# Optimization experiments

Measured on AMD Instinct MI355X. Metric: run time of the kernel, lower is better.

Reference implementation:

```python
import jax, jax.numpy as jnp
import numpy as np

SIGMA = 0.2


def setup_inputs() -> dict:
    key = jax.random.key(0)
    ks = jax.random.split(key, 16)
    N = 200000
    corner = jax.random.normal(ks[0], (N, 9), dtype=jnp.float32)
    normal = jax.random.normal(ks[1], (N, 3), dtype=jnp.float32)
    neighbour = jax.random.randint(ks[2], (N, 3), 0, N, dtype=jnp.int32)
    # Face_Rotate_Conv params: Conv1d(1,32,6,stride=3), Linear(32,64), Linear(64,64)
    conv_w = jax.random.normal(ks[3], (32, 1, 6), dtype=jnp.float32) * 0.3
    conv_b = jax.random.normal(ks[4], (32,), dtype=jnp.float32) * 0.1
    l3_w = jax.random.normal(ks[5], (64, 32), dtype=jnp.float32) * 0.15
    l3_b = jax.random.normal(ks[6], (64,), dtype=jnp.float32) * 0.05
    l4_w = jax.random.normal(ks[7], (64, 64), dtype=jnp.float32) * 0.12
    l4_b = jax.random.normal(ks[8], (64,), dtype=jnp.float32) * 0.05
    # Kernel_Correlation params: theta ~ U(0,pi), phi ~ U(0,2pi), shape [1,64,4]
    theta = jax.random.uniform(ks[9], (1, 64, 4), dtype=jnp.float32) * np.float32(np.pi)
    phi = jax.random.uniform(ks[10], (1, 64, 4), dtype=jnp.float32) * np.float32(2 * np.pi)
    # trailing 1x1 conv / bn / 1x1 conv on 131 channels
    c1_w = jax.random.normal(ks[11], (131, 131, 1), dtype=jnp.float32) * 0.08
    c1_b = jax.random.normal(ks[12], (131,), dtype=jnp.float32) * 0.05
    c2_w = jax.random.normal(ks[13], (131, 131, 1), dtype=jnp.float32) * 0.08
    c2_b = jax.random.normal(ks[14], (131,), dtype=jnp.float32) * 0.05
    bn_g = jnp.ones((131,), dtype=jnp.float32)
    bn_b = jnp.zeros((131,), dtype=jnp.float32)
    return {"corner": corner, "normal": normal, "neighbour": neighbour,
            "conv_w": conv_w, "conv_b": conv_b, "l3_w": l3_w, "l3_b": l3_b,
            "l4_w": l4_w, "l4_b": l4_b, "theta": theta, "phi": phi,
            "c1_w": c1_w, "c1_b": c1_b, "c2_w": c2_w, "c2_b": c2_b,
            "bn_g": bn_g, "bn_b": bn_b}


def reference(corner, normal, neighbour, conv_w, conv_b, l3_w, l3_b, l4_w, l4_b,
              theta, phi, c1_w, c1_b, c2_w, c2_b, bn_g, bn_b):
    # ---- Face_Rotate_Conv ----
    # cat(c1,c2,c3,c1) -> [n,12]; conv1d k=6 stride=3 over length 12 -> 3 windows
    arr = jnp.concatenate([corner[:, 0:3], corner[:, 3:6], corner[:, 6:9], corner[:, 0:3]], axis=1)
    patches = jnp.stack([arr[:, 0:6], arr[:, 3:9], arr[:, 6:12]], axis=1)  # [n,3,6]
    conv_out = jnp.einsum('npk,ok->npo', patches, conv_w[:, 0, :]) + conv_b  # [n,3,32]
    frc = conv_out.mean(axis=1)  # [n,32] (mean over output length == mean over windows)
    h = jax.nn.relu(frc @ l3_w.T + l3_b)
    x = h @ l4_w.T + l4_b  # [n,64]
    # ---- Kernel_Correlation ----
    nb = neighbour.astype(jnp.int32)
    f = jnp.stack([normal, normal[nb[:, 0]], normal[nb[:, 1]], normal[nb[:, 2]]], axis=2)  # [n,3,4]
    th, ph = theta[0], phi[0]  # [64,4]
    kern = jnp.stack([jnp.sin(th) * jnp.sin(ph), jnp.sin(th) * jnp.cos(ph), jnp.cos(th)], axis=0)  # [3,64,4]
    # ||f - k||^2 over xyz expanded via |f|^2 + |k|^2 - 2 f.k (avoids [n,3,64,4,4])
    f2 = jnp.sum(f * f, axis=1)   # [n,4]
    k2 = jnp.sum(kern * kern, axis=0)  # [64,4]
    cross = jnp.einsum('nca,cmb->nmab', f, kern)  # [n,64,4,4]
    correl = f2[:, None, :, None] + k2[None, :, None, :] - 2.0 * cross
    z = jnp.exp(correl / (-2.0 * SIGMA * SIGMA)).sum(axis=(2, 3)) / 16.0  # [n,64]
    # ---- structural_Des head ----
    feat = jnp.concatenate([normal, x, z], axis=1)  # [n,131]
    y = feat @ c1_w[:, :, 0].T + c1_b  # 1x1 conv == linear
    mu = y.mean(axis=0)
    var = y.var(axis=0)  # biased var, matches train-mode BatchNorm1d
    y = jax.nn.relu((y - mu) / jnp.sqrt(var + 1e-5) * bn_g + bn_b)
    out = y @ c2_w[:, :, 0].T + c2_b
    return out  # [n,131]
```

## Files before the change

kernel.cpp:

```cpp
#include <hip/hip_runtime.h>
#include <math.h>

typedef __attribute__((ext_vector_type(8))) short short8;
typedef _Float16 half8 __attribute__((ext_vector_type(8)));
typedef __attribute__((ext_vector_type(4))) float f32x4;
typedef __attribute__((ext_vector_type(2))) uint uint2v;
typedef unsigned int uint;
typedef unsigned short ushort;

#define N_PTS 200000
#define N_PAD 200064
#define NBLK  1563
#define NPAIR 6252
#define YST   168
#define ZK    (-18.033688011112043f)
#define C2K   (36.067376022224086f)


#define FEAT_OFF  0ull
#define WT1_OFF   118437888ull
#define WT2_OFF   118483968ull
#define KERN2_OFF 118530048ull
#define WSUM_OFF  118534144ull
#define L3H_OFF   118534528ull
#define L4H_OFF   118538624ull
#define GSUM_OFF  118546816ull
#define GSQ_OFF   118547456ull
#define SCALE_OFF 118548096ull
#define SHIFT_OFF 118548736ull

__device__ inline ushort f2h(float x) {
    return __builtin_bit_cast(ushort, (_Float16)x);
}
__device__ inline uint pack2h(float a, float b) {
    return __builtin_bit_cast(uint, __builtin_amdgcn_cvt_pkrtz(a, b));
}

__global__ void sdes_k0_setup(const float* __restrict__ conv_w, const float* __restrict__ l3w,
                              const float* __restrict__ l4w, const float* __restrict__ theta,
                              const float* __restrict__ phi, const float* __restrict__ c1w,
                              const float* __restrict__ c2w,
                              float* wsumT, ushort* l3h, ushort* l4h, float* kern2,
                              ushort* WT1t, ushort* WT2t, float* gsum, float* gsq)
{
    const int t = threadIdx.x, b = blockIdx.x;
    if (b == 90) {
        for (int i = t; i < 96; i += 256) {
            int k = i >> 5, o = i & 31;
            wsumT[k * 32 + o] = conv_w[o * 6 + k] + conv_w[o * 6 + k + 3];
        }
        for (int i = t; i < 2048; i += 256) l3h[i] = f2h(l3w[i]);
        for (int i = t; i < 4096; i += 256) l4h[i] = f2h(l4w[i]);
        int m = t >> 2, bb = t & 3;
        float th = theta[m * 4 + bb], ph = phi[m * 4 + bb];
        float st = sinf(th), ct = cosf(th), sp = sinf(ph), cp = cosf(ph);
        kern2[m * 16 + bb * 4 + 0] = st * sp * C2K;
        kern2[m * 16 + bb * 4 + 1] = st * cp * C2K;
        kern2[m * 16 + bb * 4 + 2] = ct * C2K;
        kern2[m * 16 + bb * 4 + 3] = 0.f;
        return;
    }
    if (b == 0 && t < 160) { gsum[t] = 0.f; gsq[t] = 0.f; }
    int i = b * 256 + t;
    if (i >= 144 * 160) return;
    int e = i & 7, l = (i >> 3) & 63, rem = i >> 9;
    int kc = rem % 5, tc = rem / 5;
    int n = tc * 16 + (l & 15);
    int k = kc * 32 + (l >> 4) * 8 + e;
    float v = 0.f;
    if (n < 131) {
        if (k < 64)       v = c1w[n * 131 + 3 + k];
        else if (k < 128) v = c1w[n * 131 + 67 + (k - 64)];
        else if (k < 131) v = c1w[n * 131 + (k - 128)];
    }
    WT1t[i] = f2h(v);
    float v2 = (n < 131 && k < 131) ? c2w[n * 131 + k] : 0.f;
    WT2t[i] = f2h(v2);
}

#define FST 40
#define W3T 40
#define W4T 72
__global__ __launch_bounds__(128) void sdes_k1a_mlp(
    const float* __restrict__ corner, const float* __restrict__ conv_b,
    const float* __restrict__ wsumT, const ushort* __restrict__ l3h,
    const float* __restrict__ l3b, const ushort* __restrict__ l4h,
    const float* __restrict__ l4b, ushort* __restrict__ feat)
{
    __shared__ __align__(16) ushort frcS[128 * FST];
    __shared__ __align__(16) ushort hS[128 * 64];
    __shared__ __align__(16) ushort w3S[64 * W3T];
    __shared__ __align__(16) ushort w4S[64 * W4T];
    __shared__ float wsL[96], cbL[32], b3L[64], b4L[64];
    const int t = threadIdx.x;
    for (int i = t; i < 96; i += 128) wsL[i] = wsumT[i];
    for (int i = t; i < 32; i += 128) cbL[i] = conv_b[i];
    for (int i = t; i < 64; i += 128) { b3L[i] = l3b[i]; b4L[i] = l4b[i]; }
    for (int i = t; i < 256; i += 128) {
        int c = i >> 2, kc = i & 3;
        *(uint4*)&w3S[c * W3T + kc * 8] = *(const uint4*)&l3h[c * 32 + kc * 8];
    }
    for (int i = t; i < 512; i += 128) {
        int c = i >> 3, kc = i & 7;
        *(uint4*)&w4S[c * W4T + kc * 8] = *(const uint4*)&l4h[c * 64 + kc * 8];
    }
    __syncthreads();
    {
        int row = blockIdx.x * 128 + t;
        int p = row < N_PTS ? row : N_PTS - 1;
        const float* cp = corner + (size_t)p * 9;
        float c0 = cp[0], c1 = cp[1], c2 = cp[2], c3 = cp[3], c4 = cp[4],
              c5 = cp[5], c6 = cp[6], c7 = cp[7], c8 = cp[8];
        float mp0 = (c0 + c3 + c6) * (1.f / 3.f);
        float mp1 = (c1 + c4 + c7) * (1.f / 3.f);
        float mp2 = (c2 + c5 + c8) * (1.f / 3.f);
        #pragma unroll
        for (int o = 0; o < 32; o += 2) {
            float f0 = fmaf(mp0, wsL[o], fmaf(mp1, wsL[32 + o], fmaf(mp2, wsL[64 + o], cbL[o])));
            float f1 = fmaf(mp0, wsL[o+1], fmaf(mp1, wsL[33 + o], fmaf(mp2, wsL[65 + o], cbL[o+1])));
            *(uint*)&frcS[t * FST + o] = pack2h(f0, f1);
        }
    }
    __syncthreads();

    const int lane = t & 63, w = t >> 6;
    const int rbase = w * 64;
    const int rlo = lane & 15, kg = lane >> 4;
    const f32x4 z4 = {0.f, 0.f, 0.f, 0.f};

    {
        half8 af[4], bf[4];
        #pragma unroll
        for (int rt = 0; rt < 4; ++rt)
            af[rt] = *(const half8*)&frcS[(rbase + rt * 16 + rlo) * FST + kg * 8];
        #pragma unroll
        for (int tc = 0; tc < 4; ++tc)
            bf[tc] = *(const half8*)&w3S[(tc * 16 + rlo) * W3T + kg * 8];
        #pragma unroll
        for (int rt = 0; rt < 4; ++rt) {
            #pragma unroll
            for (int tc = 0; tc < 4; ++tc) {
                f32x4 acc = __builtin_amdgcn_mfma_f32_16x16x32_f16(af[rt], bf[tc], z4, 0, 0, 0);
                int col = tc * 16 + rlo;
                float bias = b3L[col];
                #pragma unroll
                for (int r = 0; r < 4; ++r) {
                    int hrow = rbase + rt * 16 + kg * 4 + r;
                    float v = fmaxf(acc[r] + bias, 0.f);
                    int sc = (((col >> 3) ^ (hrow & 7)) << 3) | (col & 7);
                    hS[hrow * 64 + sc] = f2h(v);
                }
            }
        }
    }
    __syncthreads();

    f32x4 acc4[4][4];
    #pragma unroll
    for (int pt = 0; pt < 4; ++pt)
        #pragma unroll
        for (int tc = 0; tc < 4; ++tc) acc4[pt][tc] = z4;
    #pragma unroll
    for (int ks = 0; ks < 2; ++ks) {
        half8 af[4], bf[4];
        #pragma unroll
        for (int pt = 0; pt < 4; ++pt) {
            int row = rbase + pt * 16 + rlo;
            int blk = (ks * 4 + kg) ^ (rlo & 7);
            af[pt] = *(const half8*)&hS[row * 64 + blk * 8];
        }
        #pragma unroll
        for (int tc = 0; tc < 4; ++tc)
            bf[tc] = *(const half8*)&w4S[(tc * 16 + rlo) * W4T + ks * 32 + kg * 8];
        #pragma unroll
        for (int pt = 0; pt < 4; ++pt)
            #pragma unroll
            for (int tc = 0; tc < 4; ++tc)
                acc4[pt][tc] = __builtin_amdgcn_mfma_f32_16x16x32_f16(bf[tc], af[pt], acc4[pt][tc], 0, 0, 0);
    }
    #pragma unroll
    for (int pt = 0; pt < 4; ++pt) {
        int rtg = blockIdx.x * 8 + w * 4 + pt;
        #pragma unroll
        for (int tc = 0; tc < 4; ++tc) {
            int xb = tc * 16 + kg * 4;
            float v0 = acc4[pt][tc][0] + b4L[xb + 0];
            float v1 = acc4[pt][tc][1] + b4L[xb + 1];
            float v2 = acc4[pt][tc][2] + b4L[xb + 2];
            float v3 = acc4[pt][tc][3] + b4L[xb + 3];
            uint2v st; st.x = pack2h(v0, v1); st.y = pack2h(v2, v3);
            int kc = tc >> 1;
            int l = rlo + 16 * ((2 * tc + (kg >> 1)) & 3);
            size_t off = ((size_t)(rtg * 5 + kc)) * 512 + l * 8 + (kg & 1) * 4;
            *(uint2v*)(feat + off) = st;
        }
    }
}

__global__ __launch_bounds__(256) void sdes_k1b_z(
    const float* __restrict__ normal, const int* __restrict__ neigh,
    const float* __restrict__ kern2g, ushort* __restrict__ feat)
{
    const int t = threadIdx.x;
    const int tt = t >> 7;
    const int pi = t & 127;
    const int p0 = blockIdx.x * 128 + pi;
    const int p = p0 < N_PTS ? p0 : N_PTS - 1;
    const int rt = p0 >> 4, pl = p0 & 15;
    float f0[4], f1[4], f2v[4];
    f0[0] = normal[(size_t)p * 3 + 0]; f1[0] = normal[(size_t)p * 3 + 1]; f2v[0] = normal[(size_t)p * 3 + 2];
    #pragma unroll
    for (int a = 1; a < 4; ++a) {
        int nb = neigh[(size_t)p * 3 + (a - 1)];
        f0[a] = normal[(size_t)nb * 3 + 0];
        f1[a] = normal[(size_t)nb * 3 + 1];
        f2v[a] = normal[(size_t)nb * 3 + 2];
    }
    float base[4];
    #pragma unroll
    for (int a = 0; a < 4; ++a)
        base[a] = (f0[a]*f0[a] + f1[a]*f1[a] + f2v[a]*f2v[a] + 1.0f) * ZK;
    const size_t tbase = ((size_t)(rt * 5 + 2 + tt)) * 512;
    for (int qq = 0; qq < 4; ++qq) {
        float zv[8];
        #pragma unroll
        for (int mm = 0; mm < 8; ++mm) {
            int m = (tt * 4 + qq) * 8 + mm;
            const float* kp = kern2g + m * 16;
            float a0 = 0.f, a1 = 0.f, a2 = 0.f, a3 = 0.f;
            #pragma unroll
            for (int b = 0; b < 4; ++b) {
                float kx = kp[b * 4 + 0], ky = kp[b * 4 + 1], kz = kp[b * 4 + 2];
                a0 += __builtin_amdgcn_exp2f(fmaf(f0[0], kx, fmaf(f1[0], ky, fmaf(f2v[0], kz, base[0]))));
                a1 += __builtin_amdgcn_exp2f(fmaf(f0[1], kx, fmaf(f1[1], ky, fmaf(f2v[1], kz, base[1]))));
                a2 += __builtin_amdgcn_exp2f(fmaf(f0[2], kx, fmaf(f1[2], ky, fmaf(f2v[2], kz, base[2]))));
                a3 += __builtin_amdgcn_exp2f(fmaf(f0[3], kx, fmaf(f1[3], ky, fmaf(f2v[3], kz, base[3]))));
            }
            zv[mm] = ((a0 + a1) + (a2 + a3)) * (1.f / 16.f);
        }
        uint4 v;
        v.x = pack2h(zv[0], zv[1]); v.y = pack2h(zv[2], zv[3]);
        v.z = pack2h(zv[4], zv[5]); v.w = pack2h(zv[6], zv[7]);
        *(uint4*)(feat + tbase + (pl + 16 * qq) * 8) = v;
    }
    {
        size_t base4 = ((size_t)(rt * 5 + 4)) * 512;
        const uint4 zz = {0u, 0u, 0u, 0u};
        if (tt == 0) {
            uint4 v;
            v.x = pack2h(f0[0], f1[0]); v.y = pack2h(f2v[0], 0.f); v.z = 0u; v.w = 0u;
            *(uint4*)(feat + base4 + pl * 8) = v;
            *(uint4*)(feat + base4 + (pl + 16) * 8) = zz;
        } else {
            *(uint4*)(feat + base4 + (pl + 32) * 8) = zz;
            *(uint4*)(feat + base4 + (pl + 48) * 8) = zz;
        }
    }
}

__global__ __launch_bounds__(1024, 4) void sdes_k2_stats(
    const ushort* __restrict__ FT, const ushort* __restrict__ WT1t,
    const float* __restrict__ c1b, float* __restrict__ gsum, float* __restrict__ gsq)
{
    __shared__ __align__(16) ushort W1s[45 * 512];
    __shared__ float sS[144], sQ[144];
    const int t = threadIdx.x;
    const int lane = t & 63, wv = t >> 6;
    const int b = blockIdx.x;
    const int s = b * 16 + wv;
    const int rlo = lane & 15, kg = lane >> 4;

    const int cnt = 3 + ((wv == 0 && b < 216) ? 1 : 0);
    const int start = 3 * s + (b < 216 ? b : 216) + ((b < 216 && wv > 0) ? 1 : 0);

    half8 afA[5], afB[5];
    #pragma unroll
    for (int kc = 0; kc < 5; ++kc)
        afA[kc] = *(const half8*)(FT + ((size_t)start * 5 + kc) * 512 + lane * 8);

    for (int i = t; i < 2880; i += 1024) ((uint4*)W1s)[i] = ((const uint4*)WT1t)[i];
    if (t < 144) { sS[t] = 0.f; sQ[t] = 0.f; }
    __syncthreads();

    float sreg[9], qreg[9], bL[9];
    #pragma unroll
    for (int tc = 0; tc < 9; ++tc) {
        sreg[tc] = 0.f; qreg[tc] = 0.f;
        int n = tc * 16 + rlo;
        bL[tc] = (n < 131) ? c1b[n] : 0.f;
    }

    for (int it = 0; it < cnt; ++it) {
        const int p = start + it;
        f32x4 acc[9];
        #pragma unroll
        for (int tc = 0; tc < 9; ++tc) acc[tc] = (f32x4){0.f, 0.f, 0.f, 0.f};
        #pragma unroll
        for (int kc = 0; kc < 5; ++kc) {
            #pragma unroll
            for (int tc = 0; tc < 9; ++tc) {
                half8 bw = *(const half8*)(W1s + (tc * 5 + kc) * 512 + lane * 8);
                acc[tc] = __builtin_amdgcn_mfma_f32_16x16x32_f16(afA[kc], bw, acc[tc], 0, 0, 0);
            }
        }
        if (it + 1 < cnt) {
            #pragma unroll
            for (int kc = 0; kc < 5; ++kc)
                afB[kc] = *(const half8*)(FT + ((size_t)(p + 1) * 5 + kc) * 512 + lane * 8);
            __builtin_amdgcn_sched_barrier(0);
        }
        const int row0 = p * 16;
        #pragma unroll
        for (int tc = 0; tc < 9; ++tc) {
            float b0 = bL[tc];
            #pragma unroll
            for (int r = 0; r < 4; ++r) {
                int grow = row0 + kg * 4 + r;
                if (grow < N_PTS) {
                    float v = acc[tc][r] + b0;
                    sreg[tc] += v;
                    qreg[tc] = fmaf(v, v, qreg[tc]);
                }
            }
        }
        #pragma unroll
        for (int kc = 0; kc < 5; ++kc) afA[kc] = afB[kc];
    }

    #pragma unroll
    for (int tc = 0; tc < 9; ++tc) {
        float sv = sreg[tc], qv = qreg[tc];
        sv += __shfl_xor(sv, 16);  sv += __shfl_xor(sv, 32);
        qv += __shfl_xor(qv, 16);  qv += __shfl_xor(qv, 32);
        if (lane < 16) {
            int n = tc * 16 + rlo;
            atomicAdd(&sS[n], sv); atomicAdd(&sQ[n], qv);
        }
    }
    __syncthreads();
    if (t < 144) { atomicAdd(&gsum[t], sS[t]); atomicAdd(&gsq[t], sQ[t]); }
}

__global__ __launch_bounds__(768, 3) void sdes_k3_fused(
    const ushort* __restrict__ FT, const ushort* __restrict__ WT1t,
    const ushort* __restrict__ WT2t, const float* __restrict__ c1b,
    const float* __restrict__ gsum, const float* __restrict__ gsq,
    const float* __restrict__ bng, const float* __restrict__ bnb,
    const float* __restrict__ c2b, float* __restrict__ out)
{
    __shared__ __align__(16) ushort Ws[2 * 45 * 512];
    __shared__ __align__(16) ushort yS[192 * YST];
    __shared__ float scL[160], shL[160], b1L[160], c2L[160];
    const int t = threadIdx.x;
    const int lane = t & 63, wv = t >> 6;
    const int rlo = lane & 15, kg = lane >> 4;
    const int b = blockIdx.x;
    const int s = b * 12 + wv;

    const int cnt = 2 + ((wv == 0 && b < 108) ? 1 : 0);
    const int start = 2 * s + (b < 108 ? b : 108) + ((b < 108 && wv > 0) ? 1 : 0);

    half8 afA[5][2], afB[5][2];
    #pragma unroll
    for (int kc = 0; kc < 5; ++kc)
        #pragma unroll
        for (int pt = 0; pt < 2; ++pt)
            afA[kc][pt] = *(const half8*)(FT + ((size_t)(start * 2 + pt) * 5 + kc) * 512 + lane * 8);

    for (int i = t; i < 5760; i += 768) ((uint4*)Ws)[i] = ((const uint4*)WT1t)[i];

    if (t < 160) {
        float sc = 0.f, sh = 0.f, bb = 0.f, c2 = 0.f;
        if (t < 131) {
            float mu = gsum[t] * (1.f / 200000.f);
            float var = gsq[t] * (1.f / 200000.f) - mu * mu;
            sc = bng[t] / sqrtf(var + 1e-5f);
            sh = bnb[t] - mu * sc;
            bb = c1b[t]; c2 = c2b[t];
        }
        scL[t] = sc; shL[t] = sh; b1L[t] = bb; c2L[t] = c2;
    }
    __syncthreads();

    const half8 hz = {0, 0, 0, 0, 0, 0, 0, 0};
    ushort* slab = yS + wv * 16 * YST;

    for (int it = 0; it < cnt; ++it) {
        const int p = start + it;

        f32x4 acc[2][9];
        #pragma unroll
        for (int pt = 0; pt < 2; ++pt)
            #pragma unroll
            for (int tc = 0; tc < 9; ++tc) acc[pt][tc] = (f32x4){0.f, 0.f, 0.f, 0.f};
        #pragma unroll
        for (int kc = 0; kc < 5; ++kc) {
            #pragma unroll
            for (int tc = 0; tc < 9; ++tc) {
                half8 bw = *(const half8*)(Ws + (tc * 5 + kc) * 512 + lane * 8);
                #pragma unroll
                for (int pt = 0; pt < 2; ++pt)
                    acc[pt][tc] = __builtin_amdgcn_mfma_f32_16x16x32_f16(afA[kc][pt], bw, acc[pt][tc], 0, 0, 0);
            }
        }

        if (it + 1 < cnt) {
            #pragma unroll
            for (int kc = 0; kc < 5; ++kc)
                #pragma unroll
                for (int pt = 0; pt < 2; ++pt)
                    afB[kc][pt] = *(const half8*)(FT + ((size_t)((p + 1) * 2 + pt) * 5 + kc) * 512 + lane * 8);
            __builtin_amdgcn_sched_barrier(0);
        }

        const int row0 = p * 32;
        #pragma unroll
        for (int pt = 0; pt < 2; ++pt) {
            #pragma unroll
            for (int tc = 0; tc < 9; ++tc) {
                int n = tc * 16 + rlo;
                float sc = scL[n], sh = shL[n], bb = b1L[n];
                #pragma unroll
                for (int r = 0; r < 4; ++r) {
                    float v = fmaxf(fmaf(acc[pt][tc][r] + bb, sc, sh), 0.f);
                    slab[(kg * 4 + r) * YST + n] = f2h(v);
                }
            }

            f32x4 acc2[9];
            #pragma unroll
            for (int tc = 0; tc < 9; ++tc) acc2[tc] = (f32x4){0.f, 0.f, 0.f, 0.f};
            #pragma unroll
            for (int kc2 = 0; kc2 < 5; ++kc2) {
                bool vld = (kc2 < 4) || (kg < 2);
                half8 af2 = vld ? *(const half8*)&slab[rlo * YST + kc2 * 32 + kg * 8] : hz;
                #pragma unroll
                for (int tc = 0; tc < 9; ++tc) {
                    half8 bw = *(const half8*)(Ws + 23040 + (tc * 5 + kc2) * 512 + lane * 8);
                    acc2[tc] = __builtin_amdgcn_mfma_f32_16x16x32_f16(af2, bw, acc2[tc], 0, 0, 0);
                }
            }
            #pragma unroll
            for (int tc = 0; tc < 9; ++tc) {
                int n = tc * 16 + rlo;
                if (n < 131) {
                    float bias = c2L[n];
                    #pragma unroll
                    for (int r = 0; r < 4; ++r) {
                        int grow = row0 + pt * 16 + kg * 4 + r;
                        if (grow < N_PTS) out[(size_t)grow * 131 + n] = acc2[tc][r] + bias;
                    }
                }
            }
        }

        #pragma unroll
        for (int kc = 0; kc < 5; ++kc)
            #pragma unroll
            for (int pt = 0; pt < 2; ++pt)
                afA[kc][pt] = afB[kc][pt];
    }
}

extern "C" void kernel_launch(void* const* d_in, const int* in_sizes, int n_in,
                              void* d_out, int out_size, void* d_ws, size_t ws_size,
                              hipStream_t stream) {
    const float* corner = (const float*)d_in[0];
    const float* normal = (const float*)d_in[1];
    const int*   neigh  = (const int*)d_in[2];
    const float* conv_w = (const float*)d_in[3];
    const float* conv_b = (const float*)d_in[4];
    const float* l3_w   = (const float*)d_in[5];
    const float* l3_b   = (const float*)d_in[6];
    const float* l4_w   = (const float*)d_in[7];
    const float* l4_b   = (const float*)d_in[8];
    const float* theta  = (const float*)d_in[9];
    const float* phi    = (const float*)d_in[10];
    const float* c1_w   = (const float*)d_in[11];
    const float* c1_b   = (const float*)d_in[12];
    const float* c2_w   = (const float*)d_in[13];
    const float* c2_b   = (const float*)d_in[14];
    const float* bn_g   = (const float*)d_in[15];
    const float* bn_b   = (const float*)d_in[16];

    char* ws = (char*)d_ws;
    ushort* feat  = (ushort*)(ws + FEAT_OFF);
    ushort* WT1t  = (ushort*)(ws + WT1_OFF);
    ushort* WT2t  = (ushort*)(ws + WT2_OFF);
    float*  kern2 = (float*)(ws + KERN2_OFF);
    float*  wsumT = (float*)(ws + WSUM_OFF);
    ushort* l3h   = (ushort*)(ws + L3H_OFF);
    ushort* l4h   = (ushort*)(ws + L4H_OFF);
    float*  gsum  = (float*)(ws + GSUM_OFF);
    float*  gsq   = (float*)(ws + GSQ_OFF);

    sdes_k0_setup<<<91, 256, 0, stream>>>(conv_w, l3_w, l4_w, theta, phi, c1_w, c2_w,
                                          wsumT, l3h, l4h, kern2, WT1t, WT2t, gsum, gsq);
    sdes_k1a_mlp<<<NBLK, 128, 0, stream>>>(corner, conv_b, wsumT, l3h, l3_b, l4h, l4_b, feat);
    sdes_k1b_z<<<NBLK, 256, 0, stream>>>(normal, neigh, kern2, feat);
    sdes_k2_stats<<<256, 1024, 0, stream>>>(feat, WT1t, c1_b, gsum, gsq);
    sdes_k3_fused<<<256, 768, 0, stream>>>(feat, WT1t, WT2t, c1_b, gsum, gsq,
                                           bn_g, bn_b, c2_b, (float*)d_out);
}
```

Before: 139.1 us.

## Fuse MLP and correlation kernels, store pre-BN activations instead of recomputing first GEMM

Merges the face-MLP and kernel-correlation kernels into one 256-thread launch, with half the threads doing only the exp-based correlation while two waves run the MFMA layers. The stats kernel now writes the first linear layer's output in fp16 to a workspace buffer. The final kernel reads that buffer, applies batch norm and ReLU in registers, and runs only the second GEMM, so it no longer recomputes the first GEMM. The c2 bias is folded into the weight matrix through a constant-1 column. This trades the recomputation for roughly 64 MB of extra global write and read traffic, and y is now rounded to fp16 before normalisation.

```diff
diff --git a/kernel.cpp b/kernel.cpp
--- a/kernel.cpp
+++ b/kernel.cpp
@@ -11,8 +11,7 @@
 #define N_PTS 200000
 #define N_PAD 200064
 #define NBLK  1563
-#define NPAIR 6252
-#define YST   168
+#define YRST  160
 #define ZK    (-18.033688011112043f)
 #define C2K   (36.067376022224086f)
 
@@ -26,8 +25,7 @@
 #define L4H_OFF   118538624ull
 #define GSUM_OFF  118546816ull
 #define GSQ_OFF   118547456ull
-#define SCALE_OFF 118548096ull
-#define SHIFT_OFF 118548736ull
+#define Y_OFF     118550528ull
 
 __device__ inline ushort f2h(float x) {
     return __builtin_bit_cast(ushort, (_Float16)x);
@@ -39,7 +37,7 @@
 __global__ void sdes_k0_setup(const float* __restrict__ conv_w, const float* __restrict__ l3w,
                               const float* __restrict__ l4w, const float* __restrict__ theta,
                               const float* __restrict__ phi, const float* __restrict__ c1w,
-                              const float* __restrict__ c2w,
+                              const float* __restrict__ c2w, const float* __restrict__ c2b,
                               float* wsumT, ushort* l3h, ushort* l4h, float* kern2,
                               ushort* WT1t, ushort* WT2t, float* gsum, float* gsq)
 {
@@ -74,18 +72,24 @@
         else if (k < 131) v = c1w[n * 131 + (k - 128)];
     }
     WT1t[i] = f2h(v);
-    float v2 = (n < 131 && k < 131) ? c2w[n * 131 + k] : 0.f;
+    float v2 = 0.f;
+    if (n < 131) {
+        if (k < 131)       v2 = c2w[n * 131 + k];
+        else if (k == 144) v2 = c2b[n];
+    }
     WT2t[i] = f2h(v2);
 }
 
 #define FST 40
 #define W3T 40
 #define W4T 72
-__global__ __launch_bounds__(128) void sdes_k1a_mlp(
+__global__ __launch_bounds__(256) void sdes_k1ab(
     const float* __restrict__ corner, const float* __restrict__ conv_b,
     const float* __restrict__ wsumT, const ushort* __restrict__ l3h,
     const float* __restrict__ l3b, const ushort* __restrict__ l4h,
-    const float* __restrict__ l4b, ushort* __restrict__ feat)
+    const float* __restrict__ l4b,
+    const float* __restrict__ normal, const int* __restrict__ neigh,
+    const float* __restrict__ kern2g, ushort* __restrict__ feat)
 {
     __shared__ __align__(16) ushort frcS[128 * FST];
     __shared__ __align__(16) ushort hS[128 * 64];
@@ -93,19 +97,21 @@
     __shared__ __align__(16) ushort w4S[64 * W4T];
     __shared__ float wsL[96], cbL[32], b3L[64], b4L[64];
     const int t = threadIdx.x;
-    for (int i = t; i < 96; i += 128) wsL[i] = wsumT[i];
-    for (int i = t; i < 32; i += 128) cbL[i] = conv_b[i];
-    for (int i = t; i < 64; i += 128) { b3L[i] = l3b[i]; b4L[i] = l4b[i]; }
-    for (int i = t; i < 256; i += 128) {
+
+    for (int i = t; i < 96; i += 256) wsL[i] = wsumT[i];
+    for (int i = t; i < 32; i += 256) cbL[i] = conv_b[i];
+    for (int i = t; i < 64; i += 256) { b3L[i] = l3b[i]; b4L[i] = l4b[i]; }
+    for (int i = t; i < 256; i += 256) {
         int c = i >> 2, kc = i & 3;
         *(uint4*)&w3S[c * W3T + kc * 8] = *(const uint4*)&l3h[c * 32 + kc * 8];
     }
-    for (int i = t; i < 512; i += 128) {
+    for (int i = t; i < 512; i += 256) {
         int c = i >> 3, kc = i & 7;
         *(uint4*)&w4S[c * W4T + kc * 8] = *(const uint4*)&l4h[c * 64 + kc * 8];
     }
     __syncthreads();
-    {
+
+    if (t < 128) {
         int row = blockIdx.x * 128 + t;
         int p = row < N_PTS ? row : N_PTS - 1;
         const float* cp = corner + (size_t)p * 9;
@@ -121,14 +127,71 @@
             *(uint*)&frcS[t * FST + o] = pack2h(f0, f1);
         }
     }
+
+    {
+        const int tt = t >> 7;
+        const int pi = t & 127;
+        const int p0 = blockIdx.x * 128 + pi;
+        const int p = p0 < N_PTS ? p0 : N_PTS - 1;
+        const int rt = p0 >> 4, pl = p0 & 15;
+        float f0[4], f1[4], f2v[4];
+        f0[0] = normal[(size_t)p * 3 + 0]; f1[0] = normal[(size_t)p * 3 + 1]; f2v[0] = normal[(size_t)p * 3 + 2];
+        #pragma unroll
+        for (int a = 1; a < 4; ++a) {
+            int nb = neigh[(size_t)p * 3 + (a - 1)];
+            f0[a] = normal[(size_t)nb * 3 + 0];
+            f1[a] = normal[(size_t)nb * 3 + 1];
+            f2v[a] = normal[(size_t)nb * 3 + 2];
+        }
+        float base[4];
+        #pragma unroll
+        for (int a = 0; a < 4; ++a)
+            base[a] = (f0[a]*f0[a] + f1[a]*f1[a] + f2v[a]*f2v[a] + 1.0f) * ZK;
+        const size_t tbase = ((size_t)(rt * 5 + 2 + tt)) * 512;
+        for (int qq = 0; qq < 4; ++qq) {
+            float zv[8];
+            #pragma unroll
+            for (int mm = 0; mm < 8; ++mm) {
+                int m = (tt * 4 + qq) * 8 + mm;
+                const float* kp = kern2g + m * 16;
+                float a0 = 0.f, a1 = 0.f, a2 = 0.f, a3 = 0.f;
+                #pragma unroll
+                for (int b = 0; b < 4; ++b) {
+                    float kx = kp[b * 4 + 0], ky = kp[b * 4 + 1], kz = kp[b * 4 + 2];
+                    a0 += __builtin_amdgcn_exp2f(fmaf(f0[0], kx, fmaf(f1[0], ky, fmaf(f2v[0], kz, base[0]))));
+                    a1 += __builtin_amdgcn_exp2f(fmaf(f0[1], kx, fmaf(f1[1], ky, fmaf(f2v[1], kz, base[1]))));
+                    a2 += __builtin_amdgcn_exp2f(fmaf(f0[2], kx, fmaf(f1[2], ky, fmaf(f2v[2], kz, base[2]))));
+                    a3 += __builtin_amdgcn_exp2f(fmaf(f0[3], kx, fmaf(f1[3], ky, fmaf(f2v[3], kz, base[3]))));
+                }
+                zv[mm] = ((a0 + a1) + (a2 + a3)) * (1.f / 16.f);
+            }
+            uint4 v;
+            v.x = pack2h(zv[0], zv[1]); v.y = pack2h(zv[2], zv[3]);
+            v.z = pack2h(zv[4], zv[5]); v.w = pack2h(zv[6], zv[7]);
+            *(uint4*)(feat + tbase + (pl + 16 * qq) * 8) = v;
+        }
+        {
+            size_t base4 = ((size_t)(rt * 5 + 4)) * 512;
+            const uint4 zz = {0u, 0u, 0u, 0u};
+            if (tt == 0) {
+                uint4 v;
+                v.x = pack2h(f0[0], f1[0]); v.y = pack2h(f2v[0], 0.f); v.z = 0u; v.w = 0u;
+                *(uint4*)(feat + base4 + pl * 8) = v;
+                *(uint4*)(feat + base4 + (pl + 16) * 8) = zz;
+            } else {
+                *(uint4*)(feat + base4 + (pl + 32) * 8) = zz;
+                *(uint4*)(feat + base4 + (pl + 48) * 8) = zz;
+            }
+        }
+    }
     __syncthreads();
 
     const int lane = t & 63, w = t >> 6;
-    const int rbase = w * 64;
     const int rlo = lane & 15, kg = lane >> 4;
     const f32x4 z4 = {0.f, 0.f, 0.f, 0.f};
 
-    {
+    if (w < 2) {
+        const int rbase = w * 64;
         half8 af[4], bf[4];
         #pragma unroll
         for (int rt = 0; rt < 4; ++rt)
@@ -155,112 +218,55 @@
     }
     __syncthreads();
 
-    f32x4 acc4[4][4];
-    #pragma unroll
-    for (int pt = 0; pt < 4; ++pt)
-        #pragma unroll
-        for (int tc = 0; tc < 4; ++tc) acc4[pt][tc] = z4;
-    #pragma unroll
-    for (int ks = 0; ks < 2; ++ks) {
-        half8 af[4], bf[4];
+    if (w < 2) {
+        const int rbase = w * 64;
+        f32x4 acc4[4][4];
+        #pragma unroll
+        for (int pt = 0; pt < 4; ++pt)
+            #pragma unroll
+            for (int tc = 0; tc < 4; ++tc) acc4[pt][tc] = z4;
+        #pragma unroll
+        for (int ks = 0; ks < 2; ++ks) {
+            half8 af[4], bf[4];
+            #pragma unroll
+            for (int pt = 0; pt < 4; ++pt) {
+                int row = rbase + pt * 16 + rlo;
+                int blk = (ks * 4 + kg) ^ (rlo & 7);
+                af[pt] = *(const half8*)&hS[row * 64 + blk * 8];
+            }
+            #pragma unroll
+            for (int tc = 0; tc < 4; ++tc)
+                bf[tc] = *(const half8*)&w4S[(tc * 16 + rlo) * W4T + ks * 32 + kg * 8];
+            #pragma unroll
+            for (int pt = 0; pt < 4; ++pt)
+                #pragma unroll
+                for (int tc = 0; tc < 4; ++tc)
+                    acc4[pt][tc] = __builtin_amdgcn_mfma_f32_16x16x32_f16(bf[tc], af[pt], acc4[pt][tc], 0, 0, 0);
+        }
         #pragma unroll
         for (int pt = 0; pt < 4; ++pt) {
-            int row = rbase + pt * 16 + rlo;
-            int blk = (ks * 4 + kg) ^ (rlo & 7);
-            af[pt] = *(const half8*)&hS[row * 64 + blk * 8];
-        }
-        #pragma unroll
-        for (int tc = 0; tc < 4; ++tc)
-            bf[tc] = *(const half8*)&w4S[(tc * 16 + rlo) * W4T + ks * 32 + kg * 8];
-        #pragma unroll
-        for (int pt = 0; pt < 4; ++pt)
-            #pragma unroll
-            for (int tc = 0; tc < 4; ++tc)
-                acc4[pt][tc] = __builtin_amdgcn_mfma_f32_16x16x32_f16(bf[tc], af[pt], acc4[pt][tc], 0, 0, 0);
-    }
-    #pragma unroll
-    for (int pt = 0; pt < 4; ++pt) {
-        int rtg = blockIdx.x * 8 + w * 4 + pt;
-        #pragma unroll
-        for (int tc = 0; tc < 4; ++tc) {
-            int xb = tc * 16 + kg * 4;
-            float v0 = acc4[pt][tc][0] + b4L[xb + 0];
-            float v1 = acc4[pt][tc][1] + b4L[xb + 1];
-            float v2 = acc4[pt][tc][2] + b4L[xb + 2];
-            float v3 = acc4[pt][tc][3] + b4L[xb + 3];
-            uint2v st; st.x = pack2h(v0, v1); st.y = pack2h(v2, v3);
-            int kc = tc >> 1;
-            int l = rlo + 16 * ((2 * tc + (kg >> 1)) & 3);
-            size_t off = ((size_t)(rtg * 5 + kc)) * 512 + l * 8 + (kg & 1) * 4;
-            *(uint2v*)(feat + off) = st;
-        }
-    }
-}
-
-__global__ __launch_bounds__(256) void sdes_k1b_z(
-    const float* __restrict__ normal, const int* __restrict__ neigh,
-    const float* __restrict__ kern2g, ushort* __restrict__ feat)
-{
-    const int t = threadIdx.x;
-    const int tt = t >> 7;
-    const int pi = t & 127;
-    const int p0 = blockIdx.x * 128 + pi;
-    const int p = p0 < N_PTS ? p0 : N_PTS - 1;
-    const int rt = p0 >> 4, pl = p0 & 15;
-    float f0[4], f1[4], f2v[4];
-    f0[0] = normal[(size_t)p * 3 + 0]; f1[0] = normal[(size_t)p * 3 + 1]; f2v[0] = normal[(size_t)p * 3 + 2];
-    #pragma unroll
-    for (int a = 1; a < 4; ++a) {
-        int nb = neigh[(size_t)p * 3 + (a - 1)];
-        f0[a] = normal[(size_t)nb * 3 + 0];
-        f1[a] = normal[(size_t)nb * 3 + 1];
-        f2v[a] = normal[(size_t)nb * 3 + 2];
-    }
-    float base[4];
-    #pragma unroll
-    for (int a = 0; a < 4; ++a)
-        base[a] = (f0[a]*f0[a] + f1[a]*f1[a] + f2v[a]*f2v[a] + 1.0f) * ZK;
-    const size_t tbase = ((size_t)(rt * 5 + 2 + tt)) * 512;
-    for (int qq = 0; qq < 4; ++qq) {
-        float zv[8];
-        #pragma unroll
-        for (int mm = 0; mm < 8; ++mm) {
-            int m = (tt * 4 + qq) * 8 + mm;
-            const float* kp = kern2g + m * 16;
-            float a0 = 0.f, a1 = 0.f, a2 = 0.f, a3 = 0.f;
-            #pragma unroll
-            for (int b = 0; b < 4; ++b) {
-                float kx = kp[b * 4 + 0], ky = kp[b * 4 + 1], kz = kp[b * 4 + 2];
-                a0 += __builtin_amdgcn_exp2f(fmaf(f0[0], kx, fmaf(f1[0], ky, fmaf(f2v[0], kz, base[0]))));
-                a1 += __builtin_amdgcn_exp2f(fmaf(f0[1], kx, fmaf(f1[1], ky, fmaf(f2v[1], kz, base[1]))));
-                a2 += __builtin_amdgcn_exp2f(fmaf(f0[2], kx, fmaf(f1[2], ky, fmaf(f2v[2], kz, base[2]))));
-                a3 += __builtin_amdgcn_exp2f(fmaf(f0[3], kx, fmaf(f1[3], ky, fmaf(f2v[3], kz, base[3]))));
-            }
-            zv[mm] = ((a0 + a1) + (a2 + a3)) * (1.f / 16.f);
-        }
-        uint4 v;
-        v.x = pack2h(zv[0], zv[1]); v.y = pack2h(zv[2], zv[3]);
-        v.z = pack2h(zv[4], zv[5]); v.w = pack2h(zv[6], zv[7]);
-        *(uint4*)(feat + tbase + (pl + 16 * qq) * 8) = v;
-    }
-    {
-        size_t base4 = ((size_t)(rt * 5 + 4)) * 512;
-        const uint4 zz = {0u, 0u, 0u, 0u};
-        if (tt == 0) {
-            uint4 v;
-            v.x = pack2h(f0[0], f1[0]); v.y = pack2h(f2v[0], 0.f); v.z = 0u; v.w = 0u;
-            *(uint4*)(feat + base4 + pl * 8) = v;
-            *(uint4*)(feat + base4 + (pl + 16) * 8) = zz;
-        } else {
-            *(uint4*)(feat + base4 + (pl + 32) * 8) = zz;
-            *(uint4*)(feat + base4 + (pl + 48) * 8) = zz;
-        }
-    }
-}
-
-__global__ __launch_bounds__(1024, 4) void sdes_k2_stats(
+            int rtg = blockIdx.x * 8 + w * 4 + pt;
+            #pragma unroll
+            for (int tc = 0; tc < 4; ++tc) {
+                int xb = tc * 16 + kg * 4;
+                float v0 = acc4[pt][tc][0] + b4L[xb + 0];
+                float v1 = acc4[pt][tc][1] + b4L[xb + 1];
+                float v2 = acc4[pt][tc][2] + b4L[xb + 2];
+                float v3 = acc4[pt][tc][3] + b4L[xb + 3];
+                uint2v st; st.x = pack2h(v0, v1); st.y = pack2h(v2, v3);
+                int kc = tc >> 1;
+                int l = rlo + 16 * ((2 * tc + (kg >> 1)) & 3);
+                size_t off = ((size_t)(rtg * 5 + kc)) * 512 + l * 8 + (kg & 1) * 4;
+                *(uint2v*)(feat + off) = st;
+            }
+        }
+    }
+}
+
+__global__ __launch_bounds__(1024, 4) void sdes_k2y(
     const ushort* __restrict__ FT, const ushort* __restrict__ WT1t,
-    const float* __restrict__ c1b, float* __restrict__ gsum, float* __restrict__ gsq)
+    const float* __restrict__ c1b, float* __restrict__ gsum, float* __restrict__ gsq,
+    ushort* __restrict__ yH)
 {
     __shared__ __align__(16) ushort W1s[45 * 512];
     __shared__ float sS[144], sQ[144];
@@ -312,16 +318,24 @@
         const int row0 = p * 16;
         #pragma unroll
         for (int tc = 0; tc < 9; ++tc) {
+            const int n = tc * 16 + rlo;
             float b0 = bL[tc];
             #pragma unroll
             for (int r = 0; r < 4; ++r) {
                 int grow = row0 + kg * 4 + r;
+                float v = acc[tc][r] + b0;
+                yH[(size_t)grow * YRST + n] = f2h(v);
                 if (grow < N_PTS) {
-                    float v = acc[tc][r] + b0;
                     sreg[tc] += v;
                     qreg[tc] = fmaf(v, v, qreg[tc]);
                 }
             }
+        }
+        {
+            uint2v pz;
+            pz.x = (kg == 0) ? pack2h(1.f, 0.f) : 0u;
+            pz.y = 0u;
+            *(uint2v*)(yH + (size_t)(row0 + rlo) * YRST + 144 + kg * 4) = pz;
         }
         #pragma unroll
         for (int kc = 0; kc < 5; ++kc) afA[kc] = afB[kc];
@@ -341,124 +355,86 @@
     if (t < 144) { atomicAdd(&gsum[t], sS[t]); atomicAdd(&gsq[t], sQ[t]); }
 }
 
-__global__ __launch_bounds__(768, 3) void sdes_k3_fused(
-    const ushort* __restrict__ FT, const ushort* __restrict__ WT1t,
-    const ushort* __restrict__ WT2t, const float* __restrict__ c1b,
+__global__ __launch_bounds__(1024, 4) void sdes_k3_fused(
+    const ushort* __restrict__ yH, const ushort* __restrict__ WT2t,
     const float* __restrict__ gsum, const float* __restrict__ gsq,
     const float* __restrict__ bng, const float* __restrict__ bnb,
-    const float* __restrict__ c2b, float* __restrict__ out)
+    float* __restrict__ out)
 {
-    __shared__ __align__(16) ushort Ws[2 * 45 * 512];
-    __shared__ __align__(16) ushort yS[192 * YST];
-    __shared__ float scL[160], shL[160], b1L[160], c2L[160];
+    __shared__ __align__(16) ushort W2s[45 * 512];
+    __shared__ float scL[160], shL[160];
     const int t = threadIdx.x;
     const int lane = t & 63, wv = t >> 6;
     const int rlo = lane & 15, kg = lane >> 4;
     const int b = blockIdx.x;
-    const int s = b * 12 + wv;
-
-    const int cnt = 2 + ((wv == 0 && b < 108) ? 1 : 0);
-    const int start = 2 * s + (b < 108 ? b : 108) + ((b < 108 && wv > 0) ? 1 : 0);
-
-    half8 afA[5][2], afB[5][2];
-    #pragma unroll
-    for (int kc = 0; kc < 5; ++kc)
-        #pragma unroll
-        for (int pt = 0; pt < 2; ++pt)
-            afA[kc][pt] = *(const half8*)(FT + ((size_t)(start * 2 + pt) * 5 + kc) * 512 + lane * 8);
-
-    for (int i = t; i < 5760; i += 768) ((uint4*)Ws)[i] = ((const uint4*)WT1t)[i];
-
+    const int s = b * 16 + wv;
+
+    const int cnt = 3 + ((wv == 0 && b < 216) ? 1 : 0);
+    const int start = 3 * s + (b < 216 ? b : 216) + ((b < 216 && wv > 0) ? 1 : 0);
+
+    for (int i = t; i < 2880; i += 1024) ((uint4*)W2s)[i] = ((const uint4*)WT2t)[i];
     if (t < 160) {
-        float sc = 0.f, sh = 0.f, bb = 0.f, c2 = 0.f;
+        float sc = 0.f, sh = 0.f;
         if (t < 131) {
             float mu = gsum[t] * (1.f / 200000.f);
             float var = gsq[t] * (1.f / 200000.f) - mu * mu;
             sc = bng[t] / sqrtf(var + 1e-5f);
             sh = bnb[t] - mu * sc;
-            bb = c1b[t]; c2 = c2b[t];
-        }
-        scL[t] = sc; shL[t] = sh; b1L[t] = bb; c2L[t] = c2;
-    }
-    __syncthreads();
-
-    const half8 hz = {0, 0, 0, 0, 0, 0, 0, 0};
-    ushort* slab = yS + wv * 16 * YST;
+        } else if (t == 144) {
+            sc = 1.f;
+        }
+        scL[t] = sc; shL[t] = sh;
+    }
+    __syncthreads();
 
     for (int it = 0; it < cnt; ++it) {
-        const int p = start + it;
-
-        f32x4 acc[2][9];
-        #pragma unroll
-        for (int pt = 0; pt < 2; ++pt)
-            #pragma unroll
-            for (int tc = 0; tc < 9; ++tc) acc[pt][tc] = (f32x4){0.f, 0.f, 0.f, 0.f};
+        const int p = start + it, row0 = p * 16;
+        const int grow = row0 + rlo;
+
+        half8 yv[5];
+        #pragma unroll
+        for (int kc = 0; kc < 5; ++kc)
+            yv[kc] = *(const half8*)(yH + (size_t)grow * YRST + kc * 32 + kg * 8);
+
+        half8 af2[5];
         #pragma unroll
         for (int kc = 0; kc < 5; ++kc) {
+            const int c0 = kc * 32 + kg * 8;
+            f32x4 sA = *(const f32x4*)&scL[c0], sB = *(const f32x4*)&scL[c0 + 4];
+            f32x4 hA = *(const f32x4*)&shL[c0], hB = *(const f32x4*)&shL[c0 + 4];
+            uint4 u;
+            u.x = pack2h(fmaxf(fmaf((float)yv[kc][0], sA[0], hA[0]), 0.f),
+                         fmaxf(fmaf((float)yv[kc][1], sA[1], hA[1]), 0.f));
+            u.y = pack2h(fmaxf(fmaf((float)yv[kc][2], sA[2], hA[2]), 0.f),
+                         fmaxf(fmaf((float)yv[kc][3], sA[3], hA[3]), 0.f));
+            u.z = pack2h(fmaxf(fmaf((float)yv[kc][4], sB[0], hB[0]), 0.f),
+                         fmaxf(fmaf((float)yv[kc][5], sB[1], hB[1]), 0.f));
+            u.w = pack2h(fmaxf(fmaf((float)yv[kc][6], sB[2], hB[2]), 0.f),
+                         fmaxf(fmaf((float)yv[kc][7], sB[3], hB[3]), 0.f));
+            af2[kc] = __builtin_bit_cast(half8, u);
+        }
+
+        f32x4 acc2[9];
+        #pragma unroll
+        for (int tc = 0; tc < 9; ++tc) acc2[tc] = (f32x4){0.f, 0.f, 0.f, 0.f};
+        #pragma unroll
+        for (int kc2 = 0; kc2 < 5; ++kc2) {
             #pragma unroll
             for (int tc = 0; tc < 9; ++tc) {
-                half8 bw = *(const half8*)(Ws + (tc * 5 + kc) * 512 + lane * 8);
+                half8 bw = *(const half8*)(W2s + (tc * 5 + kc2) * 512 + lane * 8);
+                acc2[tc] = __builtin_amdgcn_mfma_f32_16x16x32_f16(bw, af2[kc2], acc2[tc], 0, 0, 0);
+            }
+        }
+
+        if (grow < N_PTS) {
+            float* op = out + (size_t)grow * 131;
+            #pragma unroll
+            for (int tc = 0; tc < 8; ++tc) {
                 #pragma unroll
-                for (int pt = 0; pt < 2; ++pt)
-                    acc[pt][tc] = __builtin_amdgcn_mfma_f32_16x16x32_f16(afA[kc][pt], bw, acc[pt][tc], 0, 0, 0);
-            }
-        }
-
-        if (it + 1 < cnt) {
-            #pragma unroll
-            for (int kc = 0; kc < 5; ++kc)
-                #pragma unroll
-                for (int pt = 0; pt < 2; ++pt)
-                    afB[kc][pt] = *(const half8*)(FT + ((size_t)((p + 1) * 2 + pt) * 5 + kc) * 512 + lane * 8);
-            __builtin_amdgcn_sched_barrier(0);
-        }
-
-        const int row0 = p * 32;
-        #pragma unroll
-        for (int pt = 0; pt < 2; ++pt) {
-            #pragma unroll
-            for (int tc = 0; tc < 9; ++tc) {
-                int n = tc * 16 + rlo;
-                float sc = scL[n], sh = shL[n], bb = b1L[n];
-                #pragma unroll
-                for (int r = 0; r < 4; ++r) {
-                    float v = fmaxf(fmaf(acc[pt][tc][r] + bb, sc, sh), 0.f);
-                    slab[(kg * 4 + r) * YST + n] = f2h(v);
-                }
-            }
-
-            f32x4 acc2[9];
-            #pragma unroll
-            for (int tc = 0; tc < 9; ++tc) acc2[tc] = (f32x4){0.f, 0.f, 0.f, 0.f};
-            #pragma unroll
-            for (int kc2 = 0; kc2 < 5; ++kc2) {
-                bool vld = (kc2 < 4) || (kg < 2);
-                half8 af2 = vld ? *(const half8*)&slab[rlo * YST + kc2 * 32 + kg * 8] : hz;
-                #pragma unroll
-                for (int tc = 0; tc < 9; ++tc) {
-                    half8 bw = *(const half8*)(Ws + 23040 + (tc * 5 + kc2) * 512 + lane * 8);
-                    acc2[tc] = __builtin_amdgcn_mfma_f32_16x16x32_f16(af2, bw, acc2[tc], 0, 0, 0);
-                }
-            }
-            #pragma unroll
-            for (int tc = 0; tc < 9; ++tc) {
-                int n = tc * 16 + rlo;
-                if (n < 131) {
-                    float bias = c2L[n];
-                    #pragma unroll
-                    for (int r = 0; r < 4; ++r) {
-                        int grow = row0 + pt * 16 + kg * 4 + r;
-                        if (grow < N_PTS) out[(size_t)grow * 131 + n] = acc2[tc][r] + bias;
-                    }
-                }
-            }
-        }
-
-        #pragma unroll
-        for (int kc = 0; kc < 5; ++kc)
-            #pragma unroll
-            for (int pt = 0; pt < 2; ++pt)
-                afA[kc][pt] = afB[kc][pt];
+                for (int r = 0; r < 4; ++r) op[tc * 16 + kg * 4 + r] = acc2[tc][r];
+            }
+            if (kg == 0) { op[128] = acc2[8][0]; op[129] = acc2[8][1]; op[130] = acc2[8][2]; }
+        }
     }
 }
 
@@ -493,12 +469,12 @@
     ushort* l4h   = (ushort*)(ws + L4H_OFF);
     float*  gsum  = (float*)(ws + GSUM_OFF);
     float*  gsq   = (float*)(ws + GSQ_OFF);
-
-    sdes_k0_setup<<<91, 256, 0, stream>>>(conv_w, l3_w, l4_w, theta, phi, c1_w, c2_w,
+    ushort* yH    = (ushort*)(ws + Y_OFF);
+
+    sdes_k0_setup<<<91, 256, 0, stream>>>(conv_w, l3_w, l4_w, theta, phi, c1_w, c2_w, c2_b,
                                           wsumT, l3h, l4h, kern2, WT1t, WT2t, gsum, gsq);
-    sdes_k1a_mlp<<<NBLK, 128, 0, stream>>>(corner, conv_b, wsumT, l3h, l3_b, l4h, l4_b, feat);
-    sdes_k1b_z<<<NBLK, 256, 0, stream>>>(normal, neigh, kern2, feat);
-    sdes_k2_stats<<<256, 1024, 0, stream>>>(feat, WT1t, c1_b, gsum, gsq);
-    sdes_k3_fused<<<256, 768, 0, stream>>>(feat, WT1t, WT2t, c1_b, gsum, gsq,
-                                           bn_g, bn_b, c2_b, (float*)d_out);
-}
+    sdes_k1ab<<<NBLK, 256, 0, stream>>>(corner, conv_b, wsumT, l3h, l3_b, l4h, l4_b,
+                                        normal, neigh, kern2, feat);
+    sdes_k2y<<<256, 1024, 0, stream>>>(feat, WT1t, c1_b, gsum, gsq, yH);
+    sdes_k3_fused<<<256, 1024, 0, stream>>>(yH, WT2t, gsum, gsq, bn_g, bn_b, (float*)d_out);
+}
```

New measurement: 329.8 us. 2.37x slower.
